# Optimization experiments

Hardware: AMD Instinct MI355X
Metric: run time of the kernel (lower is better)

Reference implementation:

```python
import jax, jax.numpy as jnp
from jax import lax
import numpy as np

STRIDE = 2
EXT_PAD = (2, 2)  # computed in __init__: (total_pad - inter_pad)//2 split symmetrically


def setup_inputs() -> dict:
    key = jax.random.key(0)
    k1, k2, k3 = jax.random.split(key, 3)
    x = jax.random.normal(k1, (32, 256, 32, 32), dtype=jnp.float32)
    # Conv kernel in OIHW layout: [out_chs, in_chs, kh, kw]
    W = jax.random.normal(k2, (128, 256, 4, 4), dtype=jnp.float32) * 0.05
    b = jax.random.normal(k3, (128,), dtype=jnp.float32) * 0.01
    return {"x": x, "W": W, "b": b}


def reference(x, W, b):
    # _Interpad: insert (stride-1) zeros between every pair of adjacent spatial
    # elements (not after the last one): new_size = (size-1)*stride + 1.
    B, C, H, Wd = x.shape
    s = STRIDE
    stuffed = jnp.zeros((B, C, (H - 1) * s + 1, (Wd - 1) * s + 1), dtype=x.dtype)
    stuffed = stuffed.at[:, :, ::s, ::s].set(x)
    # external zero padding
    p = EXT_PAD
    padded = jnp.pad(stuffed, ((0, 0), (0, 0), p, p))
    # standard (cross-correlation) conv, stride 1, dilation 1, valid padding
    y = lax.conv_general_dilated(
        padded, W,
        window_strides=(1, 1),
        padding='VALID',
        rhs_dilation=(1, 1),
        dimension_numbers=('NCHW', 'OIHW', 'NCHW'),
    )
    return y + b[None, :, None, None]
```

## Files before the change

kernel.cpp:

```cpp
#include <hip/hip_runtime.h>


typedef float  f32x4  __attribute__((ext_vector_type(4)));
typedef short  short8 __attribute__((ext_vector_type(8)));
typedef unsigned short ushort4v __attribute__((ext_vector_type(4)));
typedef unsigned short ushort8v __attribute__((ext_vector_type(8)));

__device__ __forceinline__ unsigned short f2bf(float f) {
    unsigned u = __builtin_bit_cast(unsigned, f);
    u += 0x7fffu + ((u >> 16) & 1u);
    return (unsigned short)(u >> 16);
}

__device__ __forceinline__ void ld_lds16(const unsigned short* g, unsigned short* l) {
    __builtin_amdgcn_global_load_lds(
        (const __attribute__((address_space(1))) unsigned int*)g,
        (__attribute__((address_space(3))) unsigned int*)l,
        16, 0, 0);
}

#define XP_U 288
#define XP_G 9792
#define XP_N 313344
#define WP_G 8192
#define WP_PI 262144
#define WROW 528
#define WBUFS 4224

__global__ __launch_bounds__(256) void prepack_w2(const float* __restrict__ W,
                                                  unsigned short* __restrict__ wp) {
    int t = blockIdx.x * 256 + threadIdx.x;
    int o = t >> 8, c = t & 255;
    int g = c >> 3, c8 = c & 7;
    const float4* src = (const float4*)(W + (size_t)(o * 256 + c) * 16);
    float4 q0 = src[0], q1 = src[1], q2 = src[2], q3 = src[3];
    float rows[4][4] = {{q0.x,q0.y,q0.z,q0.w},{q1.x,q1.y,q1.z,q1.w},
                        {q2.x,q2.y,q2.z,q2.w},{q3.x,q3.y,q3.z,q3.w}};
    #pragma unroll
    for (int pi = 0; pi < 2; ++pi)
    #pragma unroll
    for (int pj = 0; pj < 2; ++pj)
    #pragma unroll
    for (int du = 0; du < 2; ++du)
    #pragma unroll
    for (int dv = 0; dv < 2; ++dv)
        wp[pi*WP_PI + g*WP_G + pj*4096 + (du*2+dv)*1024 + o*8 + c8] =
            f2bf(rows[pi+2*du][pj+2*dv]);
}

__global__ __launch_bounds__(256) void prepack_x(const float* __restrict__ x,
                                                 unsigned short* __restrict__ xp) {
    __shared__ unsigned short xt[256 * 32];
    const int tid = threadIdx.x;
    const int up  = blockIdx.x;
    const int n   = blockIdx.y;
    const bool interior = (up >= 1 && up <= 32);

    if (interior) {
        const int u = up - 1;
        #pragma unroll
        for (int k = 0; k < 8; ++k) {
            int idx4 = tid + k * 256;
            int c = idx4 >> 3, v4 = idx4 & 7;
            float4 val = *(const float4*)(x + ((size_t)(n*256 + c)*32 + u)*32 + v4*4);
            ushort4v s = { f2bf(val.x), f2bf(val.y), f2bf(val.z), f2bf(val.w) };
            *(ushort4v*)&xt[c*32 + v4*4] = s;
        }
        __syncthreads();
    }

    #pragma unroll
    for (int s = 0; s < 5; ++s) {
        int id = tid + s * 256;
        if (id < 1152) {
            int g = id / 36, vp = id % 36;
            ushort8v o8 = {0,0,0,0,0,0,0,0};
            if (interior && vp >= 1 && vp <= 32) {
                #pragma unroll
                for (int e = 0; e < 8; ++e)
                    o8[e] = xt[(g*8 + e)*32 + (vp - 1)];
            }
            *(ushort8v*)&xp[(size_t)n*XP_N + g*XP_G + up*XP_U + vp*8] = o8;
        }
    }
}

__global__ __launch_bounds__(256, 3) void tconv_main(
    const unsigned short* __restrict__ xp,
    const unsigned short* __restrict__ wp,
    const float* __restrict__ bias,
    float* __restrict__ out)
{
    __shared__ __align__(16) unsigned short lds[12672];
    unsigned short* wsh0 = lds;

    const int tid  = threadIdx.x;
    const int lane = tid & 63;
    const int w    = tid >> 6;
    const int pjw  = w >> 1;
    const int half = w & 1;
    const int lg   = lane >> 4;
    const int ln   = lane & 15;
    const int du   = lg >> 1, dv = lg & 1;

    const int bid = blockIdx.x;
    const int wg  = (bid & 7) * 128 + (bid >> 3);
    const int n   = wg >> 5;
    const int rem = wg & 31;
    const int aq  = rem >> 2;
    const int pi  = (rem >> 1) & 1;
    const int oh  = rem & 1;
    const int a0  = aq * 4;

    const unsigned short* xpb = xp + (size_t)n * XP_N + (a0 + pi) * XP_U;
    const unsigned short* wpb = wp + pi * WP_PI + oh * 512;

    int xoff[4];
    #pragma unroll
    for (int jj = 0; jj < 4; ++jj) {
        int rr = half * 2 + (jj >> 1) + du;
        int vv = (jj & 1) * 16 + ln + pjw + dv;
        xoff[jj] = rr * XP_U + vv * 8;
    }
    const int wfoff = (pjw * 4 + lg) * WROW + ln * 8;

    f32x4 acc[4][4];
    #pragma unroll
    for (int i = 0; i < 4; ++i)
        #pragma unroll
        for (int jj = 0; jj < 4; ++jj)
            acc[i][jj] = (f32x4){0.f, 0.f, 0.f, 0.f};

    short8 xA[4], xB[4];

#define STAGE_W(CH, WBUF)                                                    \
    { const unsigned short* ws_ = wpb + (size_t)(CH) * WP_G;                 \
      unsigned short* wd_ = wsh0 + (WBUF) * WBUFS;                           \
      _Pragma("unroll")                                                      \
      for (int s_ = 0; s_ < 2; ++s_) {                                       \
          int r_ = w * 2 + s_;                                               \
          ld_lds16(ws_ + r_ * 1024 + lane * 8,                               \
                   wd_ + r_ * WROW + lane * 8); } }

#define LOAD_X(CH, XS)                                                      \
    { const unsigned short* xs_ = xpb + (size_t)(CH) * XP_G;                 \
      _Pragma("unroll")                                                      \
      for (int jj_ = 0; jj_ < 4; ++jj_)                                      \
          XS[jj_] = *(const short8*)(xs_ + xoff[jj_]); }

#define CHUNK(BUF, XS, CH, VMN, DO)                                          \
    {                                                                        \
        __builtin_amdgcn_sched_barrier(0);                                   \
        asm volatile("s_waitcnt vmcnt(" #VMN ")" ::: "memory");              \
        __builtin_amdgcn_s_barrier();                                        \
        __builtin_amdgcn_sched_barrier(0);                                   \
        if (DO) STAGE_W((CH) + 2, ((BUF) + 2) % 3);                          \
        const unsigned short* wb_ = wsh0 + (BUF) * WBUFS + wfoff;            \
        _Pragma("unroll")                                                    \
        for (int i_ = 0; i_ < 4; ++i_) {                                     \
            short8 av_ = *(const short8*)&wb_[i_ * 128];                     \
            _Pragma("unroll")                                                \
            for (int jj_ = 0; jj_ < 4; ++jj_)                                \
                acc[i_][jj_] = __builtin_amdgcn_mfma_f32_16x16x32_bf16(      \
                    av_, XS[jj_], acc[i_][jj_], 0, 0, 0);                    \
        }                                                                    \
        if (DO) LOAD_X((CH) + 2, XS);                                        \
    }

    STAGE_W(0, 0);
    __builtin_amdgcn_sched_barrier(0);
    LOAD_X(0, xA);
    __builtin_amdgcn_sched_barrier(0);
    STAGE_W(1, 1);
    __builtin_amdgcn_sched_barrier(0);
    LOAD_X(1, xB);
    __builtin_amdgcn_sched_barrier(0);

    for (int c6 = 0; c6 < 30; c6 += 6) {
        CHUNK(0, xA, c6 + 0, 6, 1);
        CHUNK(1, xB, c6 + 1, 6, 1);
        CHUNK(2, xA, c6 + 2, 6, 1);
        CHUNK(0, xB, c6 + 3, 6, 1);
        CHUNK(1, xA, c6 + 4, 6, 1);
        CHUNK(2, xB, c6 + 5, 6, 1);
    }
    CHUNK(0, xA, 30, 6, 0);
    CHUNK(1, xB, 31, 0, 0);

#undef CHUNK
#undef LOAD_X
#undef STAGE_W

    float* epi = (float*)lds;
    #pragma unroll
    for (int i = 0; i < 4; ++i) {
        __syncthreads();
        f32x4 bv = *(const f32x4*)&bias[oh * 64 + i * 16 + lg * 4];
        #pragma unroll
        for (int jj = 0; jj < 4; ++jj) {
            int ar = half * 2 + (jj >> 1);
            int b  = (jj & 1) * 16 + ln;
            #pragma unroll
            for (int r = 0; r < 4; ++r)
                epi[((r * 4 + lg) * 8 + ar * 2 + pjw) * 33 + b] = acc[i][jj][r] + bv[r];
        }
        __syncthreads();
        #pragma unroll
        for (int k = 0; k < 4; ++k) {
            int f    = tid + k * 256;
            int row  = f >> 4;
            int q    = f & 15;
            float2 A = *(const float2*)&epi[(row * 2 + 0) * 33 + q * 2];
            float2 B = *(const float2*)&epi[(row * 2 + 1) * 33 + q * 2];
            float4 v = { A.x, B.x, A.y, B.y };
            int olp   = row >> 2;
            int o     = oh * 64 + i * 16 + ((olp & 3) << 2) + (olp >> 2);
            int i_out = 2 * (a0 + (row & 3)) + pi;
            *(float4*)&out[(((size_t)n * 128 + o) * 64 + i_out) * 64 + q * 4] = v;
        }
    }
}

__global__ __launch_bounds__(256) void prepack_w(const float* __restrict__ W,
                                                 unsigned short* __restrict__ Wp) {
    int t = blockIdx.x * 256 + threadIdx.x;
    int o = t >> 8, c = t & 255;
    const float4* src = (const float4*)(W + (size_t)(o * 256 + c) * 16);
    float4 q0 = src[0], q1 = src[1], q2 = src[2], q3 = src[3];
    float rows[4][4] = {{q0.x,q0.y,q0.z,q0.w},{q1.x,q1.y,q1.z,q1.w},
                        {q2.x,q2.y,q2.z,q2.w},{q3.x,q3.y,q3.z,q3.w}};
    #pragma unroll
    for (int pi = 0; pi < 2; ++pi)
    #pragma unroll
    for (int pj = 0; pj < 2; ++pj)
    #pragma unroll
    for (int du = 0; du < 2; ++du)
    #pragma unroll
    for (int dv = 0; dv < 2; ++dv)
        Wp[((((pi*2+pj)*4 + du*2+dv)*128 + o)*256) + c] = f2bf(rows[pi+2*du][pj+2*dv]);
}

template<bool PRE>
__global__ __launch_bounds__(512, 2) void tconv_mfma(
    const float* __restrict__ x, const float* __restrict__ W,
    const unsigned short* __restrict__ Wp, const float* __restrict__ bias,
    float* __restrict__ out)
{
    __shared__ __align__(16) unsigned short xsh[2][9 * 34 * 8];
    __shared__ __align__(16) unsigned short wsh[2][2 * 4 * 128 * 8];

    const int tid = threadIdx.x;
    const int bid = blockIdx.x;
    const int pi  = bid & 1;
    const int aq  = (bid >> 1) & 3;
    const int n   = bid >> 3;
    const int a0  = aq * 8;
    const int u0  = a0 + pi - 1;

    const int l   = tid & 63;
    const int w   = tid >> 6;
    const int pjw = w >> 2;
    const int q   = w & 3;
    const int lg  = l >> 4;
    const int ln  = l & 15;

    const int sv = tid & 31;
    const int sg = tid >> 5;

    f32x4 acc[8][4];
    #pragma unroll
    for (int i = 0; i < 8; ++i)
        #pragma unroll
        for (int jj = 0; jj < 4; ++jj)
            acc[i][jj] = (f32x4){0.f, 0.f, 0.f, 0.f};

    float    xv[5];
    ushort4v wv[4];
    float4   wa[2], wb[2];

    auto stage_load = [&](int ch) {
        const int c0 = ch * 8;
        #pragma unroll
        for (int s = 0; s < 5; ++s) {
            int p = sg * 5 + s;
            if (p < 72) {
                int c = p & 7, rr = p >> 3;
                int u = u0 + rr;
                xv[s] = ((unsigned)u < 32u)
                      ? x[((n*256 + c0 + c)*32 + u)*32 + sv] : 0.f;
            }
        }
        if (PRE) {
            #pragma unroll
            for (int k = 0; k < 4; ++k) {
                int uu = tid + k * 512;
                int chalf = uu & 1, o = (uu >> 1) & 127;
                int sub = (uu >> 8) & 3, pjq = (uu >> 10) & 1;
                wv[k] = *(const ushort4v*)&Wp[(((pi*2 + pjq)*4 + sub)*128 + o)*256
                                              + c0 + chalf*4];
            }
        } else {
            #pragma unroll
            for (int k = 0; k < 2; ++k) {
                int pr = tid + k * 512;
                int o = pr >> 3, c = pr & 7;
                const float* base = W + ((o*256 + c0 + c) << 4) + pi*4;
                wa[k] = *(const float4*)base;
                wb[k] = *(const float4*)(base + 8);
            }
        }
    };

    auto stage_write = [&](int buf) {
        #pragma unroll
        for (int s = 0; s < 5; ++s) {
            int p = sg * 5 + s;
            if (p < 72) {
                int c = p & 7, rr = p >> 3;
                xsh[buf][(rr*34 + sv + 1)*8 + c] = f2bf(xv[s]);
            }
        }
        if (tid < 144) {
            int pr = tid >> 1;
            int rr = pr >> 3, c = pr & 7;
            int cw = (tid & 1) * 33;
            xsh[buf][(rr*34 + cw)*8 + c] = 0;
        }
        if (PRE) {
            #pragma unroll
            for (int k = 0; k < 4; ++k) {
                int uu = tid + k * 512;
                int chalf = uu & 1, o = (uu >> 1) & 127;
                int sub = (uu >> 8) & 3, pjq = (uu >> 10) & 1;
                *(ushort4v*)&wsh[buf][(((pjq*4 + sub)*128 + o)*8) + chalf*4] = wv[k];
            }
        } else {
            #pragma unroll
            for (int k = 0; k < 2; ++k) {
                int pr = tid + k * 512;
                int o = pr >> 3, c = pr & 7;
                float ra[4] = {wa[k].x, wa[k].y, wa[k].z, wa[k].w};
                float rb[4] = {wb[k].x, wb[k].y, wb[k].z, wb[k].w};
                #pragma unroll
                for (int pj2 = 0; pj2 < 2; ++pj2)
                #pragma unroll
                for (int duu = 0; duu < 2; ++duu)
                #pragma unroll
                for (int dvv = 0; dvv < 2; ++dvv) {
                    float val = duu ? rb[pj2 + 2*dvv] : ra[pj2 + 2*dvv];
                    wsh[buf][(((pj2*4 + duu*2 + dvv)*128 + o)*8) + c] = f2bf(val);
                }
            }
        }
    };

    stage_load(0);
    stage_write(0);
    __syncthreads();

    for (int ch = 0; ch < 32; ++ch) {
        const int cur = ch & 1;
        if (ch + 1 < 32) stage_load(ch + 1);

        short8 bfr[4];
        #pragma unroll
        for (int jj = 0; jj < 4; ++jj) {
            int arow = q*2 + (jj >> 1);
            int b    = (jj & 1)*16 + ln;
            int rr   = arow + (lg >> 1);
            int cw   = b + pjw + (lg & 1);
            bfr[jj]  = *(const short8*)&xsh[cur][(rr*34 + cw)*8];
        }
        #pragma unroll
        for (int i = 0; i < 8; ++i) {
            short8 av = *(const short8*)&wsh[cur][((pjw*4 + lg)*128 + i*16 + ln)*8];
            #pragma unroll
            for (int jj = 0; jj < 4; ++jj)
                acc[i][jj] = __builtin_amdgcn_mfma_f32_16x16x32_bf16(
                                 av, bfr[jj], acc[i][jj], 0, 0, 0);
        }

        if (ch + 1 < 32) stage_write(cur ^ 1);
        __syncthreads();
    }

    #pragma unroll
    for (int i = 0; i < 8; ++i) {
        const f32x4 bv = *(const f32x4*)&bias[i*16 + lg*4];
        #pragma unroll
        for (int jj = 0; jj < 4; ++jj) {
            int arow  = q*2 + (jj >> 1);
            int b     = (jj & 1)*16 + ln;
            int i_out = 2*(a0 + arow) + pi;
            int j_out = 2*b + pjw;
            int o0    = i*16 + lg*4;
            int base  = ((n*128 + o0)*64 + i_out)*64 + j_out;
            #pragma unroll
            for (int r = 0; r < 4; ++r)
                out[base + r*4096] = acc[i][jj][r] + bv[r];
        }
    }
}

extern "C" void kernel_launch(void* const* d_in, const int* in_sizes, int n_in,
                              void* d_out, int out_size, void* d_ws, size_t ws_size,
                              hipStream_t stream) {
    const float* x    = (const float*)d_in[0];
    const float* W    = (const float*)d_in[1];
    const float* bias = (const float*)d_in[2];
    float* out        = (float*)d_out;

    const size_t wp2_bytes = (size_t)2 * WP_PI * 2;
    const size_t xp_bytes  = (size_t)32 * XP_N * 2;
    if (ws_size >= wp2_bytes + xp_bytes) {
        unsigned short* wp2 = (unsigned short*)d_ws;
        unsigned short* xpp = (unsigned short*)((char*)d_ws + wp2_bytes);
        prepack_w2<<<128, 256, 0, stream>>>(W, wp2);
        prepack_x<<<dim3(34, 32), 256, 0, stream>>>(x, xpp);
        tconv_main<<<1024, 256, 0, stream>>>(xpp, wp2, bias, out);
    } else if (ws_size >= (size_t)4*4*128*256*2) {
        unsigned short* Wp = (unsigned short*)d_ws;
        prepack_w<<<128, 256, 0, stream>>>(W, Wp);
        tconv_mfma<true><<<256, 512, 0, stream>>>(x, W, Wp, bias, out);
    } else {
        tconv_mfma<false><<<256, 512, 0, stream>>>(x, W, nullptr, bias, out);
    }
}
```

Before: 63.44 us.

## Double-buffer paired weight chunks with one barrier per pair, raise occupancy

Replaces the three-buffer, one-chunk-per-barrier weight staging with a two-buffer scheme that stages two input-channel chunks at once and synchronizes once per pair. Weight rows in LDS lose their padding (528 to 512), and the activation offsets fold into a single base pointer. The launch bound rises to 4 blocks per CU. The aim is fewer barriers and more waves to hide latency. The risks are LDS bank conflicts from unpadded rows, and that the full `__syncthreads` waits on all outstanding loads, which shortens the prefetch distance.

```diff
diff --git a/kernel.cpp b/kernel.cpp
--- a/kernel.cpp
+++ b/kernel.cpp
@@ -24,8 +24,6 @@
 #define XP_N 313344
 #define WP_G 8192
 #define WP_PI 262144
-#define WROW 528
-#define WBUFS 4224
 
 __global__ __launch_bounds__(256) void prepack_w2(const float* __restrict__ W,
                                                   unsigned short* __restrict__ wp) {
@@ -85,14 +83,13 @@
     }
 }
 
-__global__ __launch_bounds__(256, 3) void tconv_main(
+__global__ __launch_bounds__(256, 4) void tconv_main(
     const unsigned short* __restrict__ xp,
     const unsigned short* __restrict__ wp,
     const float* __restrict__ bias,
     float* __restrict__ out)
 {
-    __shared__ __align__(16) unsigned short lds[12672];
-    unsigned short* wsh0 = lds;
+    __shared__ __align__(16) unsigned short lds[16384];
 
     const int tid  = threadIdx.x;
     const int lane = tid & 63;
@@ -112,17 +109,11 @@
     const int oh  = rem & 1;
     const int a0  = aq * 4;
 
-    const unsigned short* xpb = xp + (size_t)n * XP_N + (a0 + pi) * XP_U;
+    const unsigned short* xpb = xp + (size_t)n * XP_N + (a0 + pi) * XP_U
+                              + ((half * 2 + du) * XP_U + (ln + pjw + dv) * 8);
     const unsigned short* wpb = wp + pi * WP_PI + oh * 512;
 
-    int xoff[4];
-    #pragma unroll
-    for (int jj = 0; jj < 4; ++jj) {
-        int rr = half * 2 + (jj >> 1) + du;
-        int vv = (jj & 1) * 16 + ln + pjw + dv;
-        xoff[jj] = rr * XP_U + vv * 8;
-    }
-    const int wfoff = (pjw * 4 + lg) * WROW + ln * 8;
+    const int wfoff = (pjw * 4 + lg) * 512 + ln * 8;
 
     f32x4 acc[4][4];
     #pragma unroll
@@ -133,61 +124,56 @@
 
     short8 xA[4], xB[4];
 
-#define STAGE_W(CH, WBUF)                                                    \
-    { const unsigned short* ws_ = wpb + (size_t)(CH) * WP_G;                 \
-      unsigned short* wd_ = wsh0 + (WBUF) * WBUFS;                           \
-      _Pragma("unroll")                                                      \
-      for (int s_ = 0; s_ < 2; ++s_) {                                       \
-          int r_ = w * 2 + s_;                                               \
-          ld_lds16(ws_ + r_ * 1024 + lane * 8,                               \
-                   wd_ + r_ * WROW + lane * 8); } }
+#define STAGE_W(P, BUF)                                                      \
+    { _Pragma("unroll")                                                      \
+      for (int cc_ = 0; cc_ < 2; ++cc_) {                                    \
+        const unsigned short* ws_ = wpb + (size_t)(2*(P) + cc_) * WP_G;      \
+        unsigned short* wd_ = (unsigned short*)lds + (BUF)*8192 + cc_*4096;  \
+        _Pragma("unroll")                                                    \
+        for (int s_ = 0; s_ < 2; ++s_) {                                     \
+            int r_ = w * 2 + s_;                                             \
+            ld_lds16(ws_ + r_ * 1024 + lane * 8,                             \
+                     wd_ + r_ * 512 + lane * 8); } } }
 
 #define LOAD_X(CH, XS)                                                      \
     { const unsigned short* xs_ = xpb + (size_t)(CH) * XP_G;                 \
+      XS[0] = *(const short8*)(xs_);                                         \
+      XS[1] = *(const short8*)(xs_ + 128);                                   \
+      XS[2] = *(const short8*)(xs_ + XP_U);                                  \
+      XS[3] = *(const short8*)(xs_ + XP_U + 128); }
+
+#define MFMA_CHUNK(BUF, CC, XS)                                              \
+    { const unsigned short* wb_ = (unsigned short*)lds + (BUF)*8192          \
+                                  + (CC)*4096 + wfoff;                       \
       _Pragma("unroll")                                                      \
-      for (int jj_ = 0; jj_ < 4; ++jj_)                                      \
-          XS[jj_] = *(const short8*)(xs_ + xoff[jj_]); }
-
-#define CHUNK(BUF, XS, CH, VMN, DO)                                          \
-    {                                                                        \
-        __builtin_amdgcn_sched_barrier(0);                                   \
-        asm volatile("s_waitcnt vmcnt(" #VMN ")" ::: "memory");              \
-        __builtin_amdgcn_s_barrier();                                        \
-        __builtin_amdgcn_sched_barrier(0);                                   \
-        if (DO) STAGE_W((CH) + 2, ((BUF) + 2) % 3);                          \
-        const unsigned short* wb_ = wsh0 + (BUF) * WBUFS + wfoff;            \
-        _Pragma("unroll")                                                    \
-        for (int i_ = 0; i_ < 4; ++i_) {                                     \
-            short8 av_ = *(const short8*)&wb_[i_ * 128];                     \
-            _Pragma("unroll")                                                \
-            for (int jj_ = 0; jj_ < 4; ++jj_)                                \
-                acc[i_][jj_] = __builtin_amdgcn_mfma_f32_16x16x32_bf16(      \
-                    av_, XS[jj_], acc[i_][jj_], 0, 0, 0);                    \
-        }                                                                    \
-        if (DO) LOAD_X((CH) + 2, XS);                                        \
-    }
+      for (int i_ = 0; i_ < 4; ++i_) {                                       \
+          short8 av_ = *(const short8*)&wb_[i_ * 128];                       \
+          _Pragma("unroll")                                                  \
+          for (int jj_ = 0; jj_ < 4; ++jj_)                                  \
+              acc[i_][jj_] = __builtin_amdgcn_mfma_f32_16x16x32_bf16(        \
+                  av_, XS[jj_], acc[i_][jj_], 0, 0, 0);                      \
+      } }
 
     STAGE_W(0, 0);
     __builtin_amdgcn_sched_barrier(0);
     LOAD_X(0, xA);
-    __builtin_amdgcn_sched_barrier(0);
-    STAGE_W(1, 1);
-    __builtin_amdgcn_sched_barrier(0);
     LOAD_X(1, xB);
-    __builtin_amdgcn_sched_barrier(0);
-
-    for (int c6 = 0; c6 < 30; c6 += 6) {
-        CHUNK(0, xA, c6 + 0, 6, 1);
-        CHUNK(1, xB, c6 + 1, 6, 1);
-        CHUNK(2, xA, c6 + 2, 6, 1);
-        CHUNK(0, xB, c6 + 3, 6, 1);
-        CHUNK(1, xA, c6 + 4, 6, 1);
-        CHUNK(2, xB, c6 + 5, 6, 1);
-    }
-    CHUNK(0, xA, 30, 6, 0);
-    CHUNK(1, xB, 31, 0, 0);
-
-#undef CHUNK
+    __syncthreads();
+
+    for (int p = 0; p < 16; ++p) {
+        const int cur = p & 1;
+        if (p < 15) {
+            STAGE_W(p + 1, cur ^ 1);
+            __builtin_amdgcn_sched_barrier(0);
+        }
+        MFMA_CHUNK(cur, 0, xA);
+        if (p < 15) LOAD_X(2 * p + 2, xA);
+        MFMA_CHUNK(cur, 1, xB);
+        if (p < 15) LOAD_X(2 * p + 3, xB);
+        __syncthreads();
+    }
+
+#undef MFMA_CHUNK
 #undef LOAD_X
 #undef STAGE_W
 
```

New measurement: 58.11 us. 8.4% less time.
